# Optimization experiments

Measured on AMD Instinct MI355X. Metric: run time of the kernel, lower is better.

The kernel has to match this reference:

```python
import jax, jax.numpy as jnp
import numpy as np

B, T, C = 2, 2048, 1024
H, D = 16, 64
EPS = 1e-6


def _layernorm(x, gamma, beta):
    # Faithful to the torch module: uses unbiased std (Bessel) and divides by (std + eps).
    mean = x.mean(-1, keepdims=True)
    std = jnp.sqrt(jnp.sum((x - mean) ** 2, axis=-1, keepdims=True) / (x.shape[-1] - 1))
    return gamma * (x - mean) / (std + EPS) + beta


def setup_inputs() -> dict:
    key = jax.random.key(0)
    ks = jax.random.split(key, 9)
    s = lambda fan_in: 1.0 / np.sqrt(fan_in)
    return {
        "x": jax.random.normal(ks[0], (B, T, C), dtype=jnp.float32),
        "qkv_w": jax.random.uniform(ks[1], (3 * C, C), jnp.float32, -s(C), s(C)),
        "proj_w": jax.random.uniform(ks[2], (C, C), jnp.float32, -s(C), s(C)),
        "proj_b": jax.random.uniform(ks[3], (C,), jnp.float32, -s(C), s(C)),
        "l1_w": jax.random.uniform(ks[4], (4 * C, C), jnp.float32, -s(C), s(C)),
        "l1_b": jax.random.uniform(ks[5], (4 * C,), jnp.float32, -s(C), s(C)),
        "l3_w": jax.random.uniform(ks[6], (C, 4 * C), jnp.float32, -s(4 * C), s(4 * C)),
        "l3_b": jax.random.uniform(ks[7], (C,), jnp.float32, -s(4 * C), s(4 * C)),
        "ln1_g": jnp.ones((C,), jnp.float32),
        "ln1_b": jnp.zeros((C,), jnp.float32),
        "ln2_g": jnp.ones((C,), jnp.float32),
        "ln2_b": jnp.zeros((C,), jnp.float32),
    }


def _attention(x, qkv_w, proj_w, proj_b):
    Bx, Tx, Cx = x.shape
    qkv = x @ qkv_w.T                      # [B,T,3C]
    q, k, v = jnp.split(qkv, 3, axis=-1)
    q = q.reshape(Bx, Tx, H, D)
    k = k.reshape(Bx, Tx, H, D)
    v = v.reshape(Bx, Tx, H, D)
    scores = jnp.einsum("bthd,bshd->bhts", q, k) * (D ** -0.5)  # [B,H,T,T]
    causal = jnp.tril(jnp.ones((Tx, Tx), dtype=bool))
    scores = jnp.where(causal, scores, -jnp.inf)
    attn = jax.nn.softmax(scores, axis=-1)
    out = jnp.einsum("bhts,bshd->bthd", attn, v).reshape(Bx, Tx, Cx)
    return out @ proj_w.T + proj_b


def _mlp(x, l1_w, l1_b, l3_w, l3_b):
    h = jax.nn.relu(x @ l1_w.T + l1_b)     # [B,T,4C]
    return h @ l3_w.T + l3_b


def reference(x, qkv_w, proj_w, proj_b, l1_w, l1_b, l3_w, l3_b, ln1_g, ln1_b, ln2_g, ln2_b):
    # Dropout is identity in eval mode.
    x1 = x + _attention(_layernorm(x, ln1_g, ln1_b), qkv_w, proj_w, proj_b)
    x2 = x1 + _mlp(_layernorm(x1, ln2_g, ln2_b), l1_w, l1_b, l3_w, l3_b)
    return x2
```

## Files before the change

kernel.cpp:

```cpp
#include <hip/hip_runtime.h>

typedef unsigned short u16;
typedef short short8 __attribute__((ext_vector_type(8)));
typedef float floatx4 __attribute__((ext_vector_type(4)));

#define TT 2048
#define CC 1024
#define QSCALE 0.1803368801111244f
#define MFIX 32.0f

__device__ __forceinline__ u16 f2bf(float f) {
  return (u16)((__float_as_uint(f) + 0x8000u) >> 16);
}

__device__ __forceinline__ unsigned int pk2bf(float a, float b) {
  unsigned int ua = __float_as_uint(a) + 0x8000u;
  unsigned int ub = __float_as_uint(b) + 0x8000u;
  return __builtin_amdgcn_perm(ub, ua, 0x07060302u);
}

__device__ __forceinline__ void glds16(const u16* g, u16* l) {
  __builtin_amdgcn_global_load_lds((const __attribute__((address_space(1))) void*)g,
                                   (__attribute__((address_space(3))) void*)l, 16, 0, 0);
}

__device__ __forceinline__ void ln_body(const float* __restrict__ x,
                                        const float* __restrict__ g,
                                        const float* __restrict__ b,
                                        u16* __restrict__ out, int row, int tid) {
  const float4* xr = (const float4*)(x + (size_t)row * CC);
  float4 v = xr[tid];
  float s = v.x + v.y + v.z + v.w;
  float sq = v.x * v.x + v.y * v.y + v.z * v.z + v.w * v.w;
#pragma unroll
  for (int off = 1; off < 64; off <<= 1) {
    s += __shfl_xor(s, off);
    sq += __shfl_xor(sq, off);
  }
  __shared__ float ss[4], ssq[4];
  int wave = tid >> 6;
  if ((tid & 63) == 0) { ss[wave] = s; ssq[wave] = sq; }
  __syncthreads();
  s = ss[0] + ss[1] + ss[2] + ss[3];
  sq = ssq[0] + ssq[1] + ssq[2] + ssq[3];
  float mean = s * (1.0f / CC);
  float var = (sq - (float)CC * mean * mean) * (1.0f / (CC - 1));
  float inv = 1.0f / (sqrtf(fmaxf(var, 0.0f)) + 1e-6f);
  float4 gv = ((const float4*)g)[tid];
  float4 bv = ((const float4*)b)[tid];
  ushort4 o;
  o.x = f2bf(gv.x * (v.x - mean) * inv + bv.x);
  o.y = f2bf(gv.y * (v.y - mean) * inv + bv.y);
  o.z = f2bf(gv.z * (v.z - mean) * inv + bv.z);
  o.w = f2bf(gv.w * (v.w - mean) * inv + bv.w);
  ((ushort4*)(out + (size_t)row * CC))[tid] = o;
}

__global__ __launch_bounds__(256) void cvt_ln_kernel(const float* __restrict__ w0,
                                                     const float* __restrict__ w1,
                                                     const float* __restrict__ w2,
                                                     const float* __restrict__ w3,
                                                     const float* __restrict__ x,
                                                     const float* __restrict__ lg,
                                                     const float* __restrict__ lb,
                                                     u16* __restrict__ o0,
                                                     u16* __restrict__ o1,
                                                     u16* __restrict__ o2,
                                                     u16* __restrict__ o3,
                                                     u16* __restrict__ oln) {
  int blk = blockIdx.x;
  if (blk >= 12288) {
    ln_body(x, lg, lb, oln, blk - 12288, threadIdx.x);
    return;
  }
  const float* in;
  u16* out;
  int base;
  if (blk < 3072)      { in = w0; out = o0; base = 0; }
  else if (blk < 4096) { in = w1; out = o1; base = 3072; }
  else if (blk < 8192) { in = w2; out = o2; base = 4096; }
  else                 { in = w3; out = o3; base = 8192; }
  int i = (blk - base) * 256 + threadIdx.x;
  float4 v = ((const float4*)in)[i];
  ushort4 o;
  o.x = f2bf(v.x); o.y = f2bf(v.y); o.z = f2bf(v.z); o.w = f2bf(v.w);
  ((ushort4*)out)[i] = o;
}

__global__ __launch_bounds__(256) void ln_kernel(const float* __restrict__ x,
                                                 const float* __restrict__ g,
                                                 const float* __restrict__ b,
                                                 u16* __restrict__ out) {
  ln_body(x, g, b, out, blockIdx.x, threadIdx.x);
}

template <int BM, int BN, int MODE>
__global__ __launch_bounds__(256) void gemm_bt(const u16* __restrict__ A,
                                               const u16* __restrict__ W,
                                               const float* __restrict__ bias,
                                               const float* __restrict__ resid,
                                               float* __restrict__ outf,
                                               u16* __restrict__ outb,
                                               int M, int N, int K, int lda) {
  constexpr int MI = BM / 32;
  constexpr int NJ = BN / 32;
  __shared__ u16 a_lds[BM * 64];
  __shared__ u16 b_lds[BN * 64];
  int tid = threadIdx.x;
  int w = tid >> 6, lane = tid & 63;
  int l15 = lane & 15, quad = lane >> 4;
  int wm = (w >> 1) * (MI * 16), wn = (w & 1) * (NJ * 16);
  int tm = blockIdx.x * BM, tn = blockIdx.y * BN;
  size_t koff = (size_t)blockIdx.z * K;
  floatx4 acc[MI][NJ];
#pragma unroll
  for (int i = 0; i < MI; i++)
#pragma unroll
    for (int j = 0; j < NJ; j++) acc[i][j] = (floatx4){0.f, 0.f, 0.f, 0.f};

  int rsub = lane >> 3;
  int cg = (lane & 7) ^ rsub;
  const u16* Ag = A + (size_t)(tm + w * (BM / 4) + rsub) * lda + koff + cg * 8;
  const u16* Bg = W + (size_t)(tn + w * (BN / 4) + rsub) * lda + koff + cg * 8;
  u16* aL = a_lds + w * (BM / 4) * 64;
  u16* bL = b_lds + w * (BN / 4) * 64;

  int x = l15 & 7;
  int offA[MI], offB[NJ];
#pragma unroll
  for (int i = 0; i < MI; i++) offA[i] = (wm + i * 16 + l15) * 64 + ((quad ^ x) * 8);
#pragma unroll
  for (int j = 0; j < NJ; j++) offB[j] = (wn + j * 16 + l15) * 64 + ((quad ^ x) * 8);

  for (int k0 = 0; k0 < K; k0 += 64) {
    __syncthreads();
#pragma unroll
    for (int is = 0; is < BM / 32; is++) glds16(Ag + k0 + (size_t)is * 8 * lda, aL + is * 512);
#pragma unroll
    for (int is = 0; is < BN / 32; is++) glds16(Bg + k0 + (size_t)is * 8 * lda, bL + is * 512);
    __syncthreads();
#pragma unroll
    for (int s = 0; s < 2; s++) {
      short8 af[MI], bw[NJ];
#pragma unroll
      for (int i = 0; i < MI; i++) af[i] = *(const short8*)(a_lds + (offA[i] ^ (s << 5)));
#pragma unroll
      for (int j = 0; j < NJ; j++) bw[j] = *(const short8*)(b_lds + (offB[j] ^ (s << 5)));
#pragma unroll
      for (int i = 0; i < MI; i++)
#pragma unroll
        for (int j = 0; j < NJ; j++)
          acc[i][j] = __builtin_amdgcn_mfma_f32_16x16x32_bf16(af[i], bw[j], acc[i][j], 0, 0, 0);
    }
  }

  float* po = (MODE == 3) ? outf + (size_t)blockIdx.z * M * N : outf;
#pragma unroll
  for (int i = 0; i < MI; i++) {
    int row0 = tm + wm + i * 16 + quad * 4;
#pragma unroll
    for (int j = 0; j < NJ; j++) {
      int col = tn + wn + j * 16 + l15;
      float bb = (MODE == 1 || MODE == 2) ? bias[col] : 0.0f;
#pragma unroll
      for (int r = 0; r < 4; r++) {
        int row = row0 + r;
        float v = acc[i][j][r];
        if (MODE == 0) {
          if (col < 1024) v *= QSCALE;
          outb[(size_t)row * N + col] = f2bf(v);
        } else if (MODE == 1) {
          outf[(size_t)row * N + col] = v + bb + resid[(size_t)row * N + col];
        } else if (MODE == 2) {
          outb[(size_t)row * N + col] = f2bf(fmaxf(v + bb, 0.0f));
        } else {
          po[(size_t)row * N + col] = v;
        }
      }
    }
  }
}

__global__ __launch_bounds__(256) void reduce2_kernel(const float* __restrict__ p,
                                                      const float* __restrict__ bias,
                                                      const float* __restrict__ resid,
                                                      float* __restrict__ out) {
  int i = blockIdx.x * 256 + threadIdx.x;
  float4 a = ((const float4*)p)[i];
  float4 b = ((const float4*)p)[i + 1048576];
  float4 r = ((const float4*)resid)[i];
  float4 bb = ((const float4*)bias)[i & 255];
  float4 o;
  o.x = a.x + b.x + r.x + bb.x;
  o.y = a.y + b.y + r.y + bb.y;
  o.z = a.z + b.z + r.z + bb.z;
  o.w = a.w + b.w + r.w + bb.w;
  ((float4*)out)[i] = o;
}

__global__ __launch_bounds__(256) void flash_kernel(const u16* __restrict__ qkv,
                                                    u16* __restrict__ attn) {
  int bid = blockIdx.x;
  int qt = 31 - (bid >> 5);
  int bh = bid & 31;
  int b = bh >> 4, h = bh & 15;
  int tid = threadIdx.x, w = tid >> 6, lane = tid & 63;
  int l15 = lane & 15, quad = lane >> 4;

  __shared__ u16 k_lds[128 * 64];
  __shared__ u16 vt_lds[64 * 136];
  __shared__ u16 p_lds[4][16 * 136];

  int qbase = qt * 64 + w * 16;
  const u16* qp = qkv + (size_t)(b * TT + qbase + l15) * 3072 + h * 64;
  short8 qf0 = *(const short8*)(qp + quad * 8);
  short8 qf1 = *(const short8*)(qp + 32 + quad * 8);

  float l_i = 0.0f;
  floatx4 accO[4];
#pragma unroll
  for (int jf = 0; jf < 4; jf++) accO[jf] = (floatx4){0.f, 0.f, 0.f, 0.f};

  int rsub = lane >> 3;
  int cg = (lane & 7) ^ rsub;
  const u16* Kg = qkv + (size_t)(b * TT + w * 32 + rsub) * 3072 + 1024 + h * 64 + cg * 8;
  u16* kL = k_lds + w * 32 * 64;
  int s4 = (tid & 31) * 4;
  int dg = (tid >> 5) * 8;
  const u16* Vg = qkv + (size_t)(b * TT + s4) * 3072 + 2048 + h * 64 + dg;

  int x = l15 & 7;
  int kOff[8];
#pragma unroll
  for (int i = 0; i < 8; i++) kOff[i] = (i * 16 + l15) * 64 + ((quad ^ x) * 8);
  int pRd = l15 * 136 + quad * 8;

  int nt = (qt + 2) >> 1;
  for (int kt = 0; kt < nt; kt++) {
    int s0 = kt * 128;
    size_t soff = (size_t)s0 * 3072;
    uint4 R0 = *(const uint4*)(Vg + soff);
    uint4 R1 = *(const uint4*)(Vg + soff + 3072);
    uint4 R2 = *(const uint4*)(Vg + soff + 6144);
    uint4 R3 = *(const uint4*)(Vg + soff + 9216);
    __syncthreads();
#pragma unroll
    for (int is = 0; is < 4; is++) glds16(Kg + soff + (size_t)is * 8 * 3072, kL + is * 512);
    {
      unsigned int a0[4] = {R0.x, R0.y, R0.z, R0.w};
      unsigned int a1[4] = {R1.x, R1.y, R1.z, R1.w};
      unsigned int a2[4] = {R2.x, R2.y, R2.z, R2.w};
      unsigned int a3[4] = {R3.x, R3.y, R3.z, R3.w};
#pragma unroll
      for (int p = 0; p < 4; p++) {
        uint2 ev, od;
        ev.x = __builtin_amdgcn_perm(a1[p], a0[p], 0x05040100u);
        ev.y = __builtin_amdgcn_perm(a3[p], a2[p], 0x05040100u);
        od.x = __builtin_amdgcn_perm(a1[p], a0[p], 0x07060302u);
        od.y = __builtin_amdgcn_perm(a3[p], a2[p], 0x07060302u);
        *(uint2*)(vt_lds + (dg + 2 * p) * 136 + s4) = ev;
        *(uint2*)(vt_lds + (dg + 2 * p + 1) * 136 + s4) = od;
      }
    }
    __syncthreads();

    floatx4 st[8];
#pragma unroll
    for (int i = 0; i < 8; i++) st[i] = (floatx4){0.f, 0.f, 0.f, 0.f};
#pragma unroll
    for (int i = 0; i < 8; i++) {
      short8 kf0 = *(const short8*)(k_lds + kOff[i]);
      short8 kf1 = *(const short8*)(k_lds + (kOff[i] ^ 32));
      st[i] = __builtin_amdgcn_mfma_f32_16x16x32_bf16(kf0, qf0, st[i], 0, 0, 0);
      st[i] = __builtin_amdgcn_mfma_f32_16x16x32_bf16(kf1, qf1, st[i], 0, 0, 0);
    }

    if (s0 + 127 > qbase) {
      int mg = qbase + l15;
#pragma unroll
      for (int i = 0; i < 8; i++)
#pragma unroll
        for (int r = 0; r < 4; r++) {
          int s = s0 + i * 16 + quad * 4 + r;
          if (s > mg) st[i][r] = -3.0e38f;
        }
    }

    float ts = 0.0f;
#pragma unroll
    for (int i = 0; i < 8; i++)
#pragma unroll
      for (int r = 0; r < 4; r++) {
        float p = __builtin_amdgcn_exp2f(st[i][r] - MFIX);
        st[i][r] = p;
        ts += p;
      }
    ts += __shfl_xor(ts, 16);
    ts += __shfl_xor(ts, 32);
    l_i += ts;

#pragma unroll
    for (int i = 0; i < 8; i++) {
      uint2 pk;
      pk.x = pk2bf(st[i][0], st[i][1]);
      pk.y = pk2bf(st[i][2], st[i][3]);
      *(uint2*)(p_lds[w] + l15 * 136 + i * 16 + quad * 4) = pk;
    }

    short8 pf[4];
#pragma unroll
    for (int c = 0; c < 4; c++) pf[c] = *(const short8*)(p_lds[w] + pRd + c * 32);
#pragma unroll
    for (int jf = 0; jf < 4; jf++) {
      int vOff = (jf * 16 + l15) * 136 + quad * 8;
#pragma unroll
      for (int c = 0; c < 4; c++) {
        short8 vf = *(const short8*)(vt_lds + vOff + c * 32);
        accO[jf] = __builtin_amdgcn_mfma_f32_16x16x32_bf16(pf[c], vf, accO[jf], 0, 0, 0);
      }
    }
  }

  float invl = 1.0f / l_i;
  float iR[4];
#pragma unroll
  for (int r = 0; r < 4; r++) iR[r] = __shfl(invl, quad * 4 + r);
  int orow = b * TT + qbase + quad * 4;
#pragma unroll
  for (int r = 0; r < 4; r++) {
    u16* op = attn + (size_t)(orow + r) * CC + h * 64 + l15;
#pragma unroll
    for (int jf = 0; jf < 4; jf++) op[jf * 16] = f2bf(accO[jf][r] * iR[r]);
  }
}

extern "C" void kernel_launch(void* const* d_in, const int* in_sizes, int n_in,
                              void* d_out, int out_size, void* d_ws, size_t ws_size,
                              hipStream_t stream) {
  const float* x      = (const float*)d_in[0];
  const float* qkv_w  = (const float*)d_in[1];
  const float* proj_w = (const float*)d_in[2];
  const float* proj_b = (const float*)d_in[3];
  const float* l1_w   = (const float*)d_in[4];
  const float* l1_b   = (const float*)d_in[5];
  const float* l3_w   = (const float*)d_in[6];
  const float* l3_b   = (const float*)d_in[7];
  const float* ln1_g  = (const float*)d_in[8];
  const float* ln1_b  = (const float*)d_in[9];
  const float* ln2_g  = (const float*)d_in[10];
  const float* ln2_b  = (const float*)d_in[11];
  float* out = (float*)d_out;
  char* ws = (char*)d_ws;

  u16* w_qkv  = (u16*)(ws + 0);
  u16* w_proj = (u16*)(ws + 6291456);
  u16* w_l1   = (u16*)(ws + 8388608);
  u16* w_l3   = (u16*)(ws + 16777216);
  u16* lnb    = (u16*)(ws + 25165824);
  u16* qkvb   = (u16*)(ws + 33554432);
  u16* attnb  = (u16*)(ws + 58720256);
  float* x1   = (float*)(ws + 67108864);
  u16* hb     = (u16*)(ws + 83886080);
  float* l3p  = (float*)(ws + 33554432);

  cvt_ln_kernel<<<16384, 256, 0, stream>>>(qkv_w, proj_w, l1_w, l3_w, x, ln1_g, ln1_b,
                                           w_qkv, w_proj, w_l1, w_l3, lnb);
  gemm_bt<128, 128, 0><<<dim3(32, 24), 256, 0, stream>>>(lnb, w_qkv, nullptr, nullptr,
                                                         nullptr, qkvb, 4096, 3072, 1024, 1024);
  flash_kernel<<<1024, 256, 0, stream>>>(qkvb, attnb);
  gemm_bt<64, 128, 1><<<dim3(64, 8), 256, 0, stream>>>(attnb, w_proj, proj_b, x, x1,
                                                       nullptr, 4096, 1024, 1024, 1024);
  ln_kernel<<<4096, 256, 0, stream>>>(x1, ln2_g, ln2_b, lnb);
  gemm_bt<64, 128, 2><<<dim3(64, 32), 256, 0, stream>>>(lnb, w_l1, l1_b, nullptr, nullptr,
                                                        hb, 4096, 4096, 1024, 1024);
  gemm_bt<64, 128, 3><<<dim3(64, 8, 2), 256, 0, stream>>>(hb, w_l3, nullptr, nullptr, l3p,
                                                          nullptr, 4096, 1024, 2048, 4096);
  reduce2_kernel<<<4096, 256, 0, stream>>>(l3p, l3_b, x1, out);
}
```

Before: 328.8 us.

## Add 256x256-tile 4-stage pipelined GEMM for QKV and MLP-up projections

Introduces a new GEMM kernel with 256x256 output tiles, 512 threads and a 4-deep LDS ring buffer fed by direct global-to-LDS loads with swizzled offsets and explicit vmcnt waits. It replaces the 128x128 and 64x128 tiled GEMMs for the QKV projection and the first MLP layer. The aim is more data reuse per loaded tile and better overlap of memory loads with MFMA work. The trade-off is fewer blocks (192 and 256 on a 256-CU part), so the grid fills at most about one wave. Each thread also holds a large accumulator set, which raises register pressure.

```diff
diff --git a/kernel.cpp b/kernel.cpp
--- a/kernel.cpp
+++ b/kernel.cpp
@@ -181,6 +181,108 @@
   }
 }
 
+
+#define STG(st)                                                           \
+  {                                                                       \
+    const u16* gs_ = gsrc + (size_t)(st) * 32;                            \
+    u16* lb_ = &lds[(st) & 3][ldst];                                      \
+    glds16(gs_, lb_);                                                     \
+    glds16(gs_ + 16 * (size_t)K, lb_ + 512);                              \
+    glds16(gs_ + 32 * (size_t)K, lb_ + 1024);                             \
+    glds16(gs_ + 48 * (size_t)K, lb_ + 1536);                             \
+  }
+
+#define BODY(t, VM)                                                       \
+  {                                                                       \
+    asm volatile("s_waitcnt vmcnt(" #VM ")" ::: "memory");                \
+    __builtin_amdgcn_s_barrier();                                         \
+    asm volatile("" ::: "memory");                                        \
+    if ((t) + 3 < nst) STG((t) + 3);                                      \
+    const u16* Ls = &lds[(t) & 3][0];                                     \
+    short8 af[8], bf[4];                                                  \
+    _Pragma("unroll") for (int m_ = 0; m_ < 8; m_++)                      \
+        af[m_] = *(const short8*)(Ls + aOff[m_]);                         \
+    _Pragma("unroll") for (int j_ = 0; j_ < 4; j_++)                      \
+        bf[j_] = *(const short8*)(Ls + bOff[j_]);                         \
+    __builtin_amdgcn_s_setprio(1);                                        \
+    _Pragma("unroll") for (int m_ = 0; m_ < 8; m_++)                      \
+        _Pragma("unroll") for (int j_ = 0; j_ < 4; j_++)                  \
+            acc[m_][j_] = __builtin_amdgcn_mfma_f32_16x16x32_bf16(        \
+                af[m_], bf[j_], acc[m_][j_], 0, 0, 0);                    \
+    __builtin_amdgcn_s_setprio(0);                                        \
+  }
+
+template <int MODE>
+__global__ __launch_bounds__(512, 2) void gemm256(const u16* __restrict__ A,
+                                                  const u16* __restrict__ W,
+                                                  const float* __restrict__ bias,
+                                                  u16* __restrict__ outb,
+                                                  int M, int N, int K) {
+  __shared__ u16 lds[4][512 * 32];
+  const int tid = threadIdx.x;
+  const int w = tid >> 6, lane = tid & 63;
+  const int l15 = lane & 15, quad = lane >> 4;
+  const int wm = (w >> 2) * 128, wn = (w & 3) * 64;
+  const int tm = blockIdx.x * 256, tn = blockIdx.y * 256;
+
+  const int srow = lane >> 2;
+  const int xk = (lane & 3) ^ ((lane >> 4) & 3);
+  const u16* rowbase = (w < 4) ? (A + (size_t)(tm + w * 64) * K)
+                               : (W + (size_t)(tn + (w - 4) * 64) * K);
+  const u16* gsrc = rowbase + (size_t)srow * K + xk * 8;
+  const int ldst = (w * 64) * 32;
+
+  const int rx = (l15 >> 2) & 3;
+  int aOff[8], bOff[4];
+#pragma unroll
+  for (int m = 0; m < 8; m++) aOff[m] = (wm + m * 16 + l15) * 32 + ((quad ^ rx) * 8);
+#pragma unroll
+  for (int j = 0; j < 4; j++) bOff[j] = (256 + wn + j * 16 + l15) * 32 + ((quad ^ rx) * 8);
+
+  floatx4 acc[8][4];
+#pragma unroll
+  for (int m = 0; m < 8; m++)
+#pragma unroll
+    for (int j = 0; j < 4; j++) acc[m][j] = (floatx4){0.f, 0.f, 0.f, 0.f};
+
+  const int nst = K >> 5;
+
+  STG(0);
+  STG(1);
+  STG(2);
+
+#pragma unroll 4
+  for (int t = 0; t < nst - 2; ++t) BODY(t, 8);
+  BODY(nst - 2, 4);
+  BODY(nst - 1, 0);
+
+  float bb[4];
+#pragma unroll
+  for (int j = 0; j < 4; j++)
+    bb[j] = (MODE == 2) ? bias[tn + wn + j * 16 + l15] : 0.0f;
+#pragma unroll
+  for (int m = 0; m < 8; m++) {
+    int row0 = tm + wm + m * 16 + quad * 4;
+#pragma unroll
+    for (int j = 0; j < 4; j++) {
+      int col = tn + wn + j * 16 + l15;
+#pragma unroll
+      for (int r = 0; r < 4; r++) {
+        float v = acc[m][j][r];
+        if (MODE == 0) {
+          if (col < 1024) v *= QSCALE;
+          outb[(size_t)(row0 + r) * N + col] = f2bf(v);
+        } else {
+          outb[(size_t)(row0 + r) * N + col] = f2bf(fmaxf(v + bb[j], 0.0f));
+        }
+      }
+    }
+  }
+}
+
+#undef STG
+#undef BODY
+
 __global__ __launch_bounds__(256) void reduce2_kernel(const float* __restrict__ p,
                                                       const float* __restrict__ bias,
                                                       const float* __restrict__ resid,
@@ -365,14 +467,12 @@
 
   cvt_ln_kernel<<<16384, 256, 0, stream>>>(qkv_w, proj_w, l1_w, l3_w, x, ln1_g, ln1_b,
                                            w_qkv, w_proj, w_l1, w_l3, lnb);
-  gemm_bt<128, 128, 0><<<dim3(32, 24), 256, 0, stream>>>(lnb, w_qkv, nullptr, nullptr,
-                                                         nullptr, qkvb, 4096, 3072, 1024, 1024);
+  gemm256<0><<<dim3(16, 12), 512, 0, stream>>>(lnb, w_qkv, nullptr, qkvb, 4096, 3072, 1024);
   flash_kernel<<<1024, 256, 0, stream>>>(qkvb, attnb);
   gemm_bt<64, 128, 1><<<dim3(64, 8), 256, 0, stream>>>(attnb, w_proj, proj_b, x, x1,
                                                        nullptr, 4096, 1024, 1024, 1024);
   ln_kernel<<<4096, 256, 0, stream>>>(x1, ln2_g, ln2_b, lnb);
-  gemm_bt<64, 128, 2><<<dim3(64, 32), 256, 0, stream>>>(lnb, w_l1, l1_b, nullptr, nullptr,
-                                                        hb, 4096, 4096, 1024, 1024);
+  gemm256<2><<<dim3(16, 16), 512, 0, stream>>>(lnb, w_l1, l1_b, hb, 4096, 4096, 1024);
   gemm_bt<64, 128, 3><<<dim3(64, 8, 2), 256, 0, stream>>>(hb, w_l3, nullptr, nullptr, l3p,
                                                           nullptr, 4096, 1024, 2048, 4096);
   reduce2_kernel<<<4096, 256, 0, stream>>>(l3p, l3_b, x1, out);
```

Measured after the change: 316.3 us. 3.8% less time.

## Replace GEMM with 4-stage pipelined async-LDS kernel and drop split-K reduce

Applied to the files above, without the earlier changes.

Replaces the single-buffered bf16 GEMM with a new kernel that keeps a 4-deep ring of 32-wide K stages in LDS. Stages are filled by global_load_lds issued three steps ahead, synchronised with vmcnt waits and barriers, and MFMA sections get raised priority. QKV and L1 use larger 256x256 tiles on 512 threads. The split-K L3 GEMM and its separate reduce kernel are removed, with bias and residual fused into a single-pass epilogue. This should hide global load latency and cut the extra partial-sum traffic and launch, at the cost of fewer blocks for the L3 and proj GEMMs and more register and LDS pressure.

```diff
diff --git a/kernel.cpp b/kernel.cpp
--- a/kernel.cpp
+++ b/kernel.cpp
@@ -94,109 +94,134 @@
   ln_body(x, g, b, out, blockIdx.x, threadIdx.x);
 }
 
-template <int BM, int BN, int MODE>
-__global__ __launch_bounds__(256) void gemm_bt(const u16* __restrict__ A,
-                                               const u16* __restrict__ W,
-                                               const float* __restrict__ bias,
-                                               const float* __restrict__ resid,
-                                               float* __restrict__ outf,
-                                               u16* __restrict__ outb,
-                                               int M, int N, int K, int lda) {
-  constexpr int MI = BM / 32;
-  constexpr int NJ = BN / 32;
-  __shared__ u16 a_lds[BM * 64];
-  __shared__ u16 b_lds[BN * 64];
-  int tid = threadIdx.x;
-  int w = tid >> 6, lane = tid & 63;
-  int l15 = lane & 15, quad = lane >> 4;
-  int wm = (w >> 1) * (MI * 16), wn = (w & 1) * (NJ * 16);
-  int tm = blockIdx.x * BM, tn = blockIdx.y * BN;
-  size_t koff = (size_t)blockIdx.z * K;
+
+#define STGP(st, g_)                                                      \
+  glds16(gsrc + (size_t)(st) * 32 + (size_t)(g_) * 16 * K,                \
+         &lds[(st) & 3][ldst + (g_) * 512])
+
+#define BODY(t, VM)                                                       \
+  {                                                                       \
+    asm volatile("s_waitcnt vmcnt(" #VM ")" ::: "memory");                \
+    __builtin_amdgcn_s_barrier();                                         \
+    asm volatile("" ::: "memory");                                        \
+    const u16* Ls = &lds[(t) & 3][0];                                     \
+    bool stg_ = (t) + 3 < nst;                                            \
+    if (stg_) {                                                           \
+      _Pragma("unroll") for (int g_ = 0; g_ < GPP; g_++) STGP((t) + 3, g_); \
+    }                                                                     \
+    short8 bf[NJ];                                                        \
+    _Pragma("unroll") for (int j_ = 0; j_ < NJ; j_++)                     \
+        bf[j_] = *(const short8*)(Ls + bOff[j_]);                         \
+    short8 a0_ = *(const short8*)(Ls + aOff[0]);                          \
+    short8 a1_ = *(const short8*)(Ls + aOff[1]);                          \
+    __builtin_amdgcn_s_setprio(1);                                        \
+    _Pragma("unroll") for (int j_ = 0; j_ < NJ; j_++)                     \
+        acc[0][j_] = __builtin_amdgcn_mfma_f32_16x16x32_bf16(a0_, bf[j_], acc[0][j_], 0, 0, 0); \
+    _Pragma("unroll") for (int j_ = 0; j_ < NJ; j_++)                     \
+        acc[1][j_] = __builtin_amdgcn_mfma_f32_16x16x32_bf16(a1_, bf[j_], acc[1][j_], 0, 0, 0); \
+    __builtin_amdgcn_s_setprio(0);                                        \
+    _Pragma("unroll") for (int ph_ = 1; ph_ < NPH; ph_++) {               \
+      short8 c0_ = *(const short8*)(Ls + aOff[2 * ph_]);                  \
+      short8 c1_ = *(const short8*)(Ls + aOff[2 * ph_ + 1]);              \
+      if (stg_) {                                                         \
+        _Pragma("unroll") for (int g_ = 0; g_ < GPP; g_++)                \
+            STGP((t) + 3, ph_ * GPP + g_);                                \
+      }                                                                   \
+      __builtin_amdgcn_s_barrier();                                       \
+      asm volatile("" ::: "memory");                                      \
+      __builtin_amdgcn_s_setprio(1);                                      \
+      _Pragma("unroll") for (int j_ = 0; j_ < NJ; j_++)                   \
+          acc[2 * ph_][j_] = __builtin_amdgcn_mfma_f32_16x16x32_bf16(c0_, bf[j_], acc[2 * ph_][j_], 0, 0, 0); \
+      _Pragma("unroll") for (int j_ = 0; j_ < NJ; j_++)                   \
+          acc[2 * ph_ + 1][j_] = __builtin_amdgcn_mfma_f32_16x16x32_bf16(c1_, bf[j_], acc[2 * ph_ + 1][j_], 0, 0, 0); \
+      __builtin_amdgcn_s_setprio(0);                                      \
+    }                                                                     \
+  }
+
+template <int BM, int BN, int NWM, int NWN, int MODE>
+__global__ __launch_bounds__(64 * NWM * NWN, 2) void gemmp(
+    const u16* __restrict__ A, const u16* __restrict__ W,
+    const float* __restrict__ bias, const float* __restrict__ resid,
+    float* __restrict__ outf, u16* __restrict__ outb,
+    int M, int N, int K) {
+  constexpr int NW = NWM * NWN;
+  constexpr int MI = BM / NWM / 16;
+  constexpr int NJ = BN / NWN / 16;
+  constexpr int ROWS = BM + BN;
+  constexpr int NPH = MI / 2;
+  constexpr int GPP = 4 / NPH;
+  static_assert(ROWS / NW == 64, "each wave stages 64 rows");
+  __shared__ u16 lds[4][ROWS * 32];
+
+  const int tid = threadIdx.x;
+  const int w = tid >> 6, lane = tid & 63;
+  const int l15 = lane & 15, quad = lane >> 4;
+  const int wm = (w / NWN) * (MI * 16);
+  const int wn = (w % NWN) * (NJ * 16);
+  const int tm = blockIdx.x * BM, tn = blockIdx.y * BN;
+
+  const int srow = lane >> 2;
+  const int xk = (lane & 3) ^ ((lane >> 4) & 3);
+  const int wrow = w * 64;
+  const u16* rowbase = (wrow < BM) ? (A + (size_t)(tm + wrow) * K)
+                                   : (W + (size_t)(tn + wrow - BM) * K);
+  const u16* gsrc = rowbase + (size_t)srow * K + xk * 8;
+  const int ldst = wrow * 32;
+
+  const int rx = (l15 >> 2) & 3;
+  int aOff[MI], bOff[NJ];
+#pragma unroll
+  for (int m = 0; m < MI; m++) aOff[m] = (wm + m * 16 + l15) * 32 + ((quad ^ rx) * 8);
+#pragma unroll
+  for (int j = 0; j < NJ; j++) bOff[j] = (BM + wn + j * 16 + l15) * 32 + ((quad ^ rx) * 8);
+
   floatx4 acc[MI][NJ];
 #pragma unroll
-  for (int i = 0; i < MI; i++)
-#pragma unroll
-    for (int j = 0; j < NJ; j++) acc[i][j] = (floatx4){0.f, 0.f, 0.f, 0.f};
-
-  int rsub = lane >> 3;
-  int cg = (lane & 7) ^ rsub;
-  const u16* Ag = A + (size_t)(tm + w * (BM / 4) + rsub) * lda + koff + cg * 8;
-  const u16* Bg = W + (size_t)(tn + w * (BN / 4) + rsub) * lda + koff + cg * 8;
-  u16* aL = a_lds + w * (BM / 4) * 64;
-  u16* bL = b_lds + w * (BN / 4) * 64;
-
-  int x = l15 & 7;
-  int offA[MI], offB[NJ];
-#pragma unroll
-  for (int i = 0; i < MI; i++) offA[i] = (wm + i * 16 + l15) * 64 + ((quad ^ x) * 8);
-#pragma unroll
-  for (int j = 0; j < NJ; j++) offB[j] = (wn + j * 16 + l15) * 64 + ((quad ^ x) * 8);
-
-  for (int k0 = 0; k0 < K; k0 += 64) {
-    __syncthreads();
-#pragma unroll
-    for (int is = 0; is < BM / 32; is++) glds16(Ag + k0 + (size_t)is * 8 * lda, aL + is * 512);
-#pragma unroll
-    for (int is = 0; is < BN / 32; is++) glds16(Bg + k0 + (size_t)is * 8 * lda, bL + is * 512);
-    __syncthreads();
-#pragma unroll
-    for (int s = 0; s < 2; s++) {
-      short8 af[MI], bw[NJ];
-#pragma unroll
-      for (int i = 0; i < MI; i++) af[i] = *(const short8*)(a_lds + (offA[i] ^ (s << 5)));
-#pragma unroll
-      for (int j = 0; j < NJ; j++) bw[j] = *(const short8*)(b_lds + (offB[j] ^ (s << 5)));
-#pragma unroll
-      for (int i = 0; i < MI; i++)
-#pragma unroll
-        for (int j = 0; j < NJ; j++)
-          acc[i][j] = __builtin_amdgcn_mfma_f32_16x16x32_bf16(af[i], bw[j], acc[i][j], 0, 0, 0);
-    }
-  }
-
-  float* po = (MODE == 3) ? outf + (size_t)blockIdx.z * M * N : outf;
-#pragma unroll
-  for (int i = 0; i < MI; i++) {
-    int row0 = tm + wm + i * 16 + quad * 4;
+  for (int m = 0; m < MI; m++)
+#pragma unroll
+    for (int j = 0; j < NJ; j++) acc[m][j] = (floatx4){0.f, 0.f, 0.f, 0.f};
+
+  const int nst = K >> 5;
+
+#pragma unroll
+  for (int st = 0; st < 3; st++)
+#pragma unroll
+    for (int g = 0; g < 4; g++) STGP(st, g);
+
+#pragma unroll 4
+  for (int t = 0; t < nst - 2; ++t) BODY(t, 8);
+  BODY(nst - 2, 4);
+  BODY(nst - 1, 0);
+
+  float bb[NJ];
+#pragma unroll
+  for (int j = 0; j < NJ; j++)
+    bb[j] = (MODE == 1 || MODE == 2) ? bias[tn + wn + j * 16 + l15] : 0.0f;
+#pragma unroll
+  for (int m = 0; m < MI; m++) {
+    int row0 = tm + wm + m * 16 + quad * 4;
 #pragma unroll
     for (int j = 0; j < NJ; j++) {
       int col = tn + wn + j * 16 + l15;
-      float bb = (MODE == 1 || MODE == 2) ? bias[col] : 0.0f;
 #pragma unroll
       for (int r = 0; r < 4; r++) {
-        int row = row0 + r;
-        float v = acc[i][j][r];
+        float v = acc[m][j][r];
+        size_t idx = (size_t)(row0 + r) * N + col;
         if (MODE == 0) {
           if (col < 1024) v *= QSCALE;
-          outb[(size_t)row * N + col] = f2bf(v);
+          outb[idx] = f2bf(v);
         } else if (MODE == 1) {
-          outf[(size_t)row * N + col] = v + bb + resid[(size_t)row * N + col];
-        } else if (MODE == 2) {
-          outb[(size_t)row * N + col] = f2bf(fmaxf(v + bb, 0.0f));
+          outf[idx] = v + bb[j] + resid[idx];
         } else {
-          po[(size_t)row * N + col] = v;
+          outb[idx] = f2bf(fmaxf(v + bb[j], 0.0f));
         }
       }
     }
   }
 }
 
-__global__ __launch_bounds__(256) void reduce2_kernel(const float* __restrict__ p,
-                                                      const float* __restrict__ bias,
-                                                      const float* __restrict__ resid,
-                                                      float* __restrict__ out) {
-  int i = blockIdx.x * 256 + threadIdx.x;
-  float4 a = ((const float4*)p)[i];
-  float4 b = ((const float4*)p)[i + 1048576];
-  float4 r = ((const float4*)resid)[i];
-  float4 bb = ((const float4*)bias)[i & 255];
-  float4 o;
-  o.x = a.x + b.x + r.x + bb.x;
-  o.y = a.y + b.y + r.y + bb.y;
-  o.z = a.z + b.z + r.z + bb.z;
-  o.w = a.w + b.w + r.w + bb.w;
-  ((float4*)out)[i] = o;
-}
+#undef STGP
+#undef BODY
 
 __global__ __launch_bounds__(256) void flash_kernel(const u16* __restrict__ qkv,
                                                     u16* __restrict__ attn) {
@@ -361,19 +386,17 @@
   u16* attnb  = (u16*)(ws + 58720256);
   float* x1   = (float*)(ws + 67108864);
   u16* hb     = (u16*)(ws + 83886080);
-  float* l3p  = (float*)(ws + 33554432);
 
   cvt_ln_kernel<<<16384, 256, 0, stream>>>(qkv_w, proj_w, l1_w, l3_w, x, ln1_g, ln1_b,
                                            w_qkv, w_proj, w_l1, w_l3, lnb);
-  gemm_bt<128, 128, 0><<<dim3(32, 24), 256, 0, stream>>>(lnb, w_qkv, nullptr, nullptr,
-                                                         nullptr, qkvb, 4096, 3072, 1024, 1024);
+  gemmp<256, 256, 2, 4, 0><<<dim3(16, 12), 512, 0, stream>>>(
+      lnb, w_qkv, nullptr, nullptr, nullptr, qkvb, 4096, 3072, 1024);
   flash_kernel<<<1024, 256, 0, stream>>>(qkvb, attnb);
-  gemm_bt<64, 128, 1><<<dim3(64, 8), 256, 0, stream>>>(attnb, w_proj, proj_b, x, x1,
-                                                       nullptr, 4096, 1024, 1024, 1024);
+  gemmp<128, 128, 2, 2, 1><<<dim3(32, 8), 256, 0, stream>>>(
+      attnb, w_proj, proj_b, x, x1, nullptr, 4096, 1024, 1024);
   ln_kernel<<<4096, 256, 0, stream>>>(x1, ln2_g, ln2_b, lnb);
-  gemm_bt<64, 128, 2><<<dim3(64, 32), 256, 0, stream>>>(lnb, w_l1, l1_b, nullptr, nullptr,
-                                                        hb, 4096, 4096, 1024, 1024);
-  gemm_bt<64, 128, 3><<<dim3(64, 8, 2), 256, 0, stream>>>(hb, w_l3, nullptr, nullptr, l3p,
-                                                          nullptr, 4096, 1024, 2048, 4096);
-  reduce2_kernel<<<4096, 256, 0, stream>>>(l3p, l3_b, x1, out);
-}
+  gemmp<256, 256, 2, 4, 2><<<dim3(16, 16), 512, 0, stream>>>(
+      lnb, w_l1, l1_b, nullptr, nullptr, hb, 4096, 4096, 1024);
+  gemmp<128, 128, 2, 2, 1><<<dim3(32, 8), 256, 0, stream>>>(
+      hb, w_l3, l3_b, x1, out, nullptr, 4096, 1024, 4096);
+}
```

New measurement: 312.8 us. -4.9%, faster.
